# Optimization experiments

Measured on AMD Instinct MI355X. Metric: run time of the kernel, lower is better.

The kernel has to match this reference:

```python
import jax, jax.numpy as jnp
import numpy as np

B, L, D = 2, 256, 256  # batch, length, raw feature dim (W dims are D+1)

def setup_inputs() -> dict:
    key = jax.random.key(0)
    k1, k2, k3, kw = jax.random.split(key, 4)
    layer1 = jax.random.normal(k1, (B, L, D), dtype=jnp.float32)
    layer2 = jax.random.normal(k2, (B, L, D), dtype=jnp.float32)
    layer3 = jax.random.normal(k3, (B, L, D), dtype=jnp.float32)
    # xavier_normal_ for a 3D tensor: fan_in = D+1 * (D+1) receptive? torch treats
    # dim0 as fan_out-ish; we just use a matched-scale gaussian (correctness of the
    # contraction math is what matters for the kernel baseline).
    std = float(np.sqrt(2.0 / ((D + 1) + (D + 1) * (D + 1))))
    W = jax.random.normal(kw, (D + 1, D + 1, D + 1), dtype=jnp.float32) * std
    return {"layer1": layer1, "layer2": layer2, "layer3": layer3, "W": W}

def _append_ones(x):
    ones = jnp.ones(x.shape[:2] + (1,), dtype=x.dtype)
    return jnp.concatenate([x, ones], axis=-1)

def reference(layer1, layer2, layer3, W):
    l1 = _append_ones(layer1)  # [n, L, a]
    l2 = _append_ones(layer2)  # [n, L, b]
    l3 = _append_ones(layer3)  # [n, L, c]
    # Chained contraction: nia,abc -> nibc ; nibc,njb -> nijc ; nijc,nkc -> nijk
    t = jnp.einsum('nia,abc->nibc', l1, W)
    t = jnp.einsum('nibc,njb->nijc', t, l2)
    out = jnp.einsum('nijc,nkc->nijk', t, l3)
    return out
```

## Files before the change

kernel.cpp:

```cpp
#include <hip/hip_runtime.h>

typedef unsigned short u16;
typedef __attribute__((ext_vector_type(8))) short bf16x8;
typedef __attribute__((ext_vector_type(4))) float f32x4;

#define GLOAD_LDS16(gsrc, ldst)                                               \
  __builtin_amdgcn_global_load_lds(                                           \
      (const __attribute__((address_space(1))) void*)(gsrc),                  \
      (__attribute__((address_space(3))) void*)(ldst), 16, 0, 0)

#define LDSOFF(p) \
  ((unsigned)(uintptr_t)(__attribute__((address_space(3))) const void*)(p))

#define SB0 __builtin_amdgcn_sched_barrier(0)

__device__ __forceinline__ u16 f2bf(float x) {
  unsigned u = __float_as_uint(x);
  u = (u + 0x7FFFu + ((u >> 16) & 1u)) >> 16;
  return (u16)u;
}

__global__ void prep_l_kernel(const float* __restrict__ l1,
                              const float* __restrict__ l2,
                              const float* __restrict__ l3,
                              u16* __restrict__ o1, u16* __restrict__ o2,
                              u16* __restrict__ o3) {
  int idx = blockIdx.x * 256 + threadIdx.x;
  const int NR = 512 * 288;
  if (idx >= 3 * NR) return;
  int which = idx / NR, rem = idx - which * NR;
  int r = rem / 288, p = rem - r * 288;
  const float* s = which == 0 ? l1 : which == 1 ? l2 : l3;
  u16* d = which == 0 ? o1 : which == 1 ? o2 : o3;
  float v = (p < 256) ? s[r * 256 + p] : (p == 256 ? 1.0f : 0.0f);
  d[rem] = f2bf(v);
}

__global__ void prep_w_kernel(const float* __restrict__ W, u16* __restrict__ W2) {
  __shared__ float tile[32][33];
  const int a0 = blockIdx.x * 32, c0 = blockIdx.y * 32, b = blockIdx.z;
  const int t = threadIdx.x;
#pragma unroll
  for (int p = 0; p < 4; ++p) {
    int idx = t + p * 256;
    int cl = idx & 31, r = idx >> 5;
    int a = a0 + r, c = c0 + cl;
    float v = 0.0f;
    if (a < 257 && b < 257 && c < 257) v = W[((long)a * 257 + b) * 257 + c];
    tile[r][cl] = v;
  }
  __syncthreads();
#pragma unroll
  for (int p = 0; p < 4; ++p) {
    int idx = t + p * 256;
    int al = idx & 31, ccl = idx >> 5;
    W2[((long)(c0 + ccl) * 288 + b) * 288 + (a0 + al)] = f2bf(tile[al][ccl]);
  }
}

__global__ __launch_bounds__(256, 4) void gemm_nt(
    const u16* __restrict__ A, const u16* __restrict__ B, u16* __restrict__ C,
    int K, int lda, int ldb, int ldc) {
  __shared__ u16 As[2][4096];
  __shared__ u16 Bs[2][4096];
  const int t = threadIdx.x;
  const int bid = blockIdx.x;
  const int xcd = bid & 7, sq = bid >> 3;
  const int nt = xcd * 81 + (sq >> 2);
  const int mt = sq & 3;
  const int m0 = mt * 128, n0 = nt * 128;
  const int lane = t & 63;
  const int w = t >> 6;
  const int wr = (w >> 1) * 64, wc = (w & 1) * 64;
  const int r16 = lane & 15;
  const int cgrp = lane >> 4;
  const int rr = cgrp * 4;
  const unsigned ABase = LDSOFF(&As[0][0]);
  const unsigned BBase = LDSOFF(&Bs[0][0]);
  (void)K;

  const u16* PA = A + (long)m0 * lda;
  const u16* PB = B + (long)n0 * ldb;

#define STG(buf, k0)                                                          \
  {                                                                           \
    _Pragma("unroll") for (int _p = 0; _p < 2; ++_p) {                        \
      int _q = t + _p * 256;                                                  \
      int _r = _q >> 2, _g = (_q & 3) ^ ((_r >> 1) & 3);                      \
      GLOAD_LDS16(PA + (long)_r * lda + (k0) + _g * 8, &As[buf][_q * 8]);     \
      GLOAD_LDS16(PB + (long)_r * ldb + (k0) + _g * 8, &Bs[buf][_q * 8]);     \
    }                                                                         \
  }

  f32x4 acc[4][4];
  const f32x4 zero = {0.f, 0.f, 0.f, 0.f};
#pragma unroll
  for (int i = 0; i < 4; ++i)
#pragma unroll
    for (int j = 0; j < 4; ++j) acc[i][j] = zero;

  STG(0, 0);

#define GCOL(NI)                                                              \
  __builtin_amdgcn_s_setprio(1);                                              \
  acc[0][NI] = __builtin_amdgcn_mfma_f32_16x16x32_bf16(af[0], bf[NI], acc[0][NI], 0, 0, 0); \
  acc[1][NI] = __builtin_amdgcn_mfma_f32_16x16x32_bf16(af[1], bf[NI], acc[1][NI], 0, 0, 0); \
  acc[2][NI] = __builtin_amdgcn_mfma_f32_16x16x32_bf16(af[2], bf[NI], acc[2][NI], 0, 0, 0); \
  acc[3][NI] = __builtin_amdgcn_mfma_f32_16x16x32_bf16(af[3], bf[NI], acc[3][NI], 0, 0, 0); \
  __builtin_amdgcn_s_setprio(0);                                              \
  SB0;

#define GSTEP(KS, NW)                                                         \
  {                                                                           \
    if ((KS) < 8) STG(((KS) + 1) & 1, ((KS) + 1) * 32);                       \
    asm volatile("s_waitcnt vmcnt(" #NW ")" ::: "memory");                    \
    SB0;                                                                      \
    __builtin_amdgcn_s_barrier();                                             \
    SB0;                                                                      \
    bf16x8 af[4], bf[4];                                                      \
    _Pragma("unroll") for (int mi = 0; mi < 4; ++mi) {                        \
      int R = wr + mi * 16 + r16;                                             \
      unsigned ao = ABase + (unsigned)(((((KS) & 1) * 4096) + R * 32 +        \
                                       ((cgrp ^ ((R >> 1) & 3)) * 8)) * 2);   \
      asm volatile("ds_read_b128 %0, %1" : "=v"(af[mi]) : "v"(ao));           \
    }                                                                         \
    _Pragma("unroll") for (int ni = 0; ni < 4; ++ni) {                        \
      int R = wc + ni * 16 + r16;                                             \
      unsigned ao = BBase + (unsigned)(((((KS) & 1) * 4096) + R * 32 +        \
                                       ((cgrp ^ ((R >> 1) & 3)) * 8)) * 2);   \
      asm volatile("ds_read_b128 %0, %1" : "=v"(bf[ni]) : "v"(ao));           \
    }                                                                         \
    SB0;                                                                      \
    asm volatile("s_waitcnt lgkmcnt(3)" ::: "memory"); SB0;                   \
    GCOL(0)                                                                   \
    asm volatile("s_waitcnt lgkmcnt(2)" ::: "memory"); SB0;                   \
    GCOL(1)                                                                   \
    asm volatile("s_waitcnt lgkmcnt(1)" ::: "memory"); SB0;                   \
    GCOL(2)                                                                   \
    asm volatile("s_waitcnt lgkmcnt(0)" ::: "memory"); SB0;                   \
    GCOL(3)                                                                   \
  }

  GSTEP(0, 4) GSTEP(1, 4) GSTEP(2, 4) GSTEP(3, 4) GSTEP(4, 4)
  GSTEP(5, 4) GSTEP(6, 4) GSTEP(7, 4) GSTEP(8, 0)
#undef GSTEP
#undef GCOL
#undef STG

#pragma unroll
  for (int mi = 0; mi < 4; ++mi) {
    int gm = m0 + wr + mi * 16 + rr;
#pragma unroll
    for (int ni = 0; ni < 4; ++ni) {
      int gc = n0 + wc + ni * 16 + r16;
#pragma unroll
      for (int r = 0; r < 4; ++r)
        C[(long)(gm + r) * ldc + gc] = f2bf(acc[mi][ni][r]);
    }
  }
}

__global__ __launch_bounds__(512, 2) void fused23(
    const u16* __restrict__ l2b, const u16* __restrict__ l3b,
    const u16* __restrict__ T1, float* __restrict__ out) {
  __shared__ u16 S[128 * 296];
  __shared__ u16 Bst[4][288 * 32];
  const int t = threadIdx.x;
  const int lane = t & 63;
  const int w = t >> 6;

  const int bid = blockIdx.x;
  const int xcd = bid & 7;
  const int seq = bid >> 3;
  const int ni = xcd * 64 + (seq >> 1);
  const int half = seq & 1;
  const int n = ni >> 8;

  const int r16 = lane & 15;
  const int cgrp = lane >> 4;
  const int kb = cgrp * 8;
  const int rr = cgrp * 4;
  const f32x4 zero = {0.f, 0.f, 0.f, 0.f};

  const u16* A2 = l2b + (long)n * 73728 + (long)(half * 128) * 288;
  const u16* BT = T1 + (long)ni * 82944;
  const u16* B3 = l3b + (long)n * 73728;
  const unsigned BOF = LDSOFF(&Bst[0][0]);
  const unsigned SOF = LDSOFF(&S[0]);

#define ISSUE_A(buf, kk)                                                      \
  {                                                                           \
    int q1 = w * 144 + lane;                                                  \
    int r1 = q1 >> 2, g1 = (q1 & 3) ^ ((r1 >> 1) & 3);                        \
    GLOAD_LDS16(BT + (long)r1 * 288 + (kk) * 32 + g1 * 8, &Bst[(buf)][q1 * 8]); \
    int q2 = q1 + 64;                                                         \
    int r2 = q2 >> 2, g2 = (q2 & 3) ^ ((r2 >> 1) & 3);                        \
    GLOAD_LDS16(BT + (long)r2 * 288 + (kk) * 32 + g2 * 8, &Bst[(buf)][q2 * 8]); \
    if (lane < 16) {                                                          \
      int q3 = w * 144 + 128 + lane;                                          \
      int r3 = q3 >> 2, g3 = (q3 & 3) ^ ((r3 >> 1) & 3);                      \
      GLOAD_LDS16(BT + (long)r3 * 288 + (kk) * 32 + g3 * 8, &Bst[(buf)][q3 * 8]); \
    }                                                                         \
  }
#define ISSUE_B(buf, kk)                                                      \
  {                                                                           \
    int q1 = w * 128 + lane;                                                  \
    int r1 = q1 >> 2, g1 = (q1 & 3) ^ ((r1 >> 1) & 3);                        \
    GLOAD_LDS16(B3 + (long)r1 * 288 + (kk) * 32 + g1 * 8, &Bst[(buf)][q1 * 8]); \
    int q2 = q1 + 64;                                                         \
    int r2 = q2 >> 2, g2 = (q2 & 3) ^ ((r2 >> 1) & 3);                        \
    GLOAD_LDS16(B3 + (long)r2 * 288 + (kk) * 32 + g2 * 8, &Bst[(buf)][q2 * 8]); \
  }

  {
    const int wm = w & 3, wn = w >> 2;
    f32x4 acc[2][9];
#pragma unroll
    for (int i = 0; i < 2; ++i)
#pragma unroll
      for (int j = 0; j < 9; ++j) acc[i][j] = zero;

    bf16x8 afr[18];
#pragma unroll
    for (int k = 0; k < 9; ++k)
#pragma unroll
      for (int mi = 0; mi < 2; ++mi)
        afr[k * 2 + mi] = *(const bf16x8*)(A2 +
            (long)(wm * 32 + mi * 16 + r16) * 288 + k * 32 + kb);
    SB0;

    ISSUE_A(0, 0);
    ISSUE_A(1, 1);

#define FA_MM(NJ)                                                             \
  __builtin_amdgcn_s_setprio(1);                                              \
  acc[0][NJ] = __builtin_amdgcn_mfma_f32_16x16x32_bf16(afc0, bf[NJ], acc[0][NJ], 0, 0, 0); \
  acc[1][NJ] = __builtin_amdgcn_mfma_f32_16x16x32_bf16(afc1, bf[NJ], acc[1][NJ], 0, 0, 0); \
  __builtin_amdgcn_s_setprio(0);

#define FA_STEP(K, NW)                                                        \
  {                                                                           \
    if ((K) + 2 <= 8) ISSUE_A(((K) + 2) & 3, (K) + 2);                        \
    asm volatile("s_waitcnt vmcnt(" #NW ")" ::: "memory");                    \
    SB0;                                                                      \
    __builtin_amdgcn_s_barrier();                                             \
    SB0;                                                                      \
    bf16x8 bf[9];                                                             \
    _Pragma("unroll") for (int nj = 0; nj < 9; ++nj) {                        \
      const int R = wn * 144 + nj * 16 + r16;                                 \
      unsigned ao = BOF + (unsigned)((((K) & 3) * 9216 + R * 32 +             \
                                      ((cgrp ^ ((R >> 1) & 3)) * 8)) * 2);    \
      asm volatile("ds_read_b128 %0, %1" : "=v"(bf[nj]) : "v"(ao));           \
    }                                                                         \
    SB0;                                                                      \
    const bf16x8 afc0 = afr[(K) * 2 + 0], afc1 = afr[(K) * 2 + 1];            \
    asm volatile("s_waitcnt lgkmcnt(6)" ::: "memory"); SB0;                   \
    FA_MM(0) FA_MM(1) FA_MM(2) SB0;                                           \
    asm volatile("s_waitcnt lgkmcnt(3)" ::: "memory"); SB0;                   \
    FA_MM(3) FA_MM(4) FA_MM(5) SB0;                                           \
    asm volatile("s_waitcnt lgkmcnt(0)" ::: "memory"); SB0;                   \
    FA_MM(6) FA_MM(7) FA_MM(8) SB0;                                           \
  }
    FA_STEP(0, 6) FA_STEP(1, 6) FA_STEP(2, 6) FA_STEP(3, 6) FA_STEP(4, 6)
    FA_STEP(5, 6) FA_STEP(6, 6) FA_STEP(7, 3) FA_STEP(8, 0)
#undef FA_STEP
#undef FA_MM

    __syncthreads();
    ISSUE_B(0, 0);
    ISSUE_B(1, 1);
#pragma unroll
    for (int mi = 0; mi < 2; ++mi)
#pragma unroll
      for (int nj = 0; nj < 9; ++nj)
#pragma unroll
        for (int q = 0; q < 4; ++q)
          S[(wm * 32 + mi * 16 + rr + q) * 296 + wn * 144 + nj * 16 + r16] =
              f2bf(acc[mi][nj][q]);
  }
  __syncthreads();

  {
    const int wm = w & 1, wn = w >> 1;
    f32x4 acc[4][4];
#pragma unroll
    for (int i = 0; i < 4; ++i)
#pragma unroll
      for (int j = 0; j < 4; ++j) acc[i][j] = zero;

#define FB_MM(NI)                                                             \
  __builtin_amdgcn_s_setprio(1);                                              \
  acc[0][NI] = __builtin_amdgcn_mfma_f32_16x16x32_bf16(af[0], bf[NI], acc[0][NI], 0, 0, 0); \
  acc[1][NI] = __builtin_amdgcn_mfma_f32_16x16x32_bf16(af[1], bf[NI], acc[1][NI], 0, 0, 0); \
  acc[2][NI] = __builtin_amdgcn_mfma_f32_16x16x32_bf16(af[2], bf[NI], acc[2][NI], 0, 0, 0); \
  acc[3][NI] = __builtin_amdgcn_mfma_f32_16x16x32_bf16(af[3], bf[NI], acc[3][NI], 0, 0, 0); \
  __builtin_amdgcn_s_setprio(0);                                              \
  SB0;

#define FB_STEP(K, NW)                                                        \
  {                                                                           \
    if ((K) + 2 <= 8) ISSUE_B(((K) + 2) & 3, (K) + 2);                        \
    asm volatile("s_waitcnt vmcnt(" #NW ")" ::: "memory");                    \
    SB0;                                                                      \
    __builtin_amdgcn_s_barrier();                                             \
    SB0;                                                                      \
    bf16x8 af[4], bf[4];                                                      \
    _Pragma("unroll") for (int mi = 0; mi < 4; ++mi) {                        \
      unsigned ao = SOF + (unsigned)(((wm * 64 + mi * 16 + r16) * 296 +       \
                                      (K) * 32 + kb) * 2);                    \
      asm volatile("ds_read_b128 %0, %1" : "=v"(af[mi]) : "v"(ao));           \
    }                                                                         \
    _Pragma("unroll") for (int nj = 0; nj < 4; ++nj) {                        \
      const int R = wn * 64 + nj * 16 + r16;                                  \
      unsigned ao = BOF + (unsigned)((((K) & 3) * 9216 + R * 32 +             \
                                      ((cgrp ^ ((R >> 1) & 3)) * 8)) * 2);    \
      asm volatile("ds_read_b128 %0, %1" : "=v"(bf[nj]) : "v"(ao));           \
    }                                                                         \
    SB0;                                                                      \
    asm volatile("s_waitcnt lgkmcnt(3)" ::: "memory"); SB0;                   \
    FB_MM(0)                                                                  \
    asm volatile("s_waitcnt lgkmcnt(2)" ::: "memory"); SB0;                   \
    FB_MM(1)                                                                  \
    asm volatile("s_waitcnt lgkmcnt(1)" ::: "memory"); SB0;                   \
    FB_MM(2)                                                                  \
    asm volatile("s_waitcnt lgkmcnt(0)" ::: "memory"); SB0;                   \
    FB_MM(3)                                                                  \
  }
    FB_STEP(0, 4) FB_STEP(1, 4) FB_STEP(2, 4) FB_STEP(3, 4) FB_STEP(4, 4)
    FB_STEP(5, 4) FB_STEP(6, 4) FB_STEP(7, 2) FB_STEP(8, 0)
#undef FB_STEP
#undef FB_MM

    float* O = out + (long)ni * 65536 + (long)(half * 128 + wm * 64) * 256 + wn * 64;
#pragma unroll
    for (int mi = 0; mi < 4; ++mi)
#pragma unroll
      for (int nj = 0; nj < 4; ++nj)
#pragma unroll
        for (int q = 0; q < 4; ++q)
          O[(long)(mi * 16 + rr + q) * 256 + nj * 16 + r16] = acc[mi][nj][q];
  }
#undef ISSUE_A
#undef ISSUE_B
}

extern "C" void kernel_launch(void* const* d_in, const int* in_sizes, int n_in,
                              void* d_out, int out_size, void* d_ws, size_t ws_size,
                              hipStream_t stream) {
  const float* l1 = (const float*)d_in[0];
  const float* l2 = (const float*)d_in[1];
  const float* l3 = (const float*)d_in[2];
  const float* W = (const float*)d_in[3];
  float* out = (float*)d_out;
  char* ws = (char*)d_ws;

  const long LB = 512L * 288 * 2;
  u16* l1b = (u16*)ws;
  u16* l2b = (u16*)(ws + LB);
  u16* l3b = (u16*)(ws + 2 * LB);
  u16* T1 = (u16*)(ws + 3 * LB);
  u16* W2 = (u16*)d_out;

  prep_l_kernel<<<1728, 256, 0, stream>>>(l1, l2, l3, l1b, l2b, l3b);

  dim3 gw(9, 9, 288);
  prep_w_kernel<<<gw, 256, 0, stream>>>(W, W2);

  gemm_nt<<<2592, 256, 0, stream>>>(l1b, W2, T1, 288, 288, 288, 82944);

  fused23<<<1024, 512, 0, stream>>>(l2b, l3b, T1, out);
}
```

Baseline: 159.1 us.

## Enlarge gemm_nt tiles to 256x256 with 512 threads and reorder prefetch

The first GEMM now uses 256x256 output tiles computed by 8 waves, each producing a 128x64 sub-tile. This doubles operand reuse per LDS load and cuts the grid from 2592 to 648 blocks. The next k-slice prefetch is now issued after the current slice's LDS reads, with a full vmcnt(0) wait at the top of each step. The trade-offs are more accumulator registers, larger LDS buffers, fewer blocks for load balance, and less overlap between global loads and compute.

```diff
diff --git a/kernel.cpp b/kernel.cpp
--- a/kernel.cpp
+++ b/kernel.cpp
@@ -58,20 +58,21 @@
   }
 }
 
-__global__ __launch_bounds__(256, 4) void gemm_nt(
+__global__ __launch_bounds__(512, 2) void gemm_nt(
     const u16* __restrict__ A, const u16* __restrict__ B, u16* __restrict__ C,
     int K, int lda, int ldb, int ldc) {
-  __shared__ u16 As[2][4096];
-  __shared__ u16 Bs[2][4096];
+  __shared__ u16 As[2][8192];
+  __shared__ u16 Bs[2][8192];
   const int t = threadIdx.x;
   const int bid = blockIdx.x;
-  const int xcd = bid & 7, sq = bid >> 3;
-  const int nt = xcd * 81 + (sq >> 2);
-  const int mt = sq & 3;
-  const int m0 = mt * 128, n0 = nt * 128;
+  const int xcd = bid & 7, s = bid >> 3;
+  const int g = xcd * 81 + s;
+  const int mt = g & 1, nt = g >> 1;
+  const int m0 = mt * 256, n0 = nt * 256;
   const int lane = t & 63;
   const int w = t >> 6;
-  const int wr = (w >> 1) * 64, wc = (w & 1) * 64;
+  const int wm = w >> 2;
+  const int wn = w & 3;
   const int r16 = lane & 15;
   const int cgrp = lane >> 4;
   const int rr = cgrp * 4;
@@ -85,17 +86,17 @@
 #define STG(buf, k0)                                                          \
   {                                                                           \
     _Pragma("unroll") for (int _p = 0; _p < 2; ++_p) {                        \
-      int _q = t + _p * 256;                                                  \
+      int _q = t + _p * 512;                                                  \
       int _r = _q >> 2, _g = (_q & 3) ^ ((_r >> 1) & 3);                      \
       GLOAD_LDS16(PA + (long)_r * lda + (k0) + _g * 8, &As[buf][_q * 8]);     \
       GLOAD_LDS16(PB + (long)_r * ldb + (k0) + _g * 8, &Bs[buf][_q * 8]);     \
     }                                                                         \
   }
 
-  f32x4 acc[4][4];
+  f32x4 acc[8][4];
   const f32x4 zero = {0.f, 0.f, 0.f, 0.f};
 #pragma unroll
-  for (int i = 0; i < 4; ++i)
+  for (int i = 0; i < 8; ++i)
 #pragma unroll
     for (int j = 0; j < 4; ++j) acc[i][j] = zero;
 
@@ -103,33 +104,33 @@
 
 #define GCOL(NI)                                                              \
   __builtin_amdgcn_s_setprio(1);                                              \
-  acc[0][NI] = __builtin_amdgcn_mfma_f32_16x16x32_bf16(af[0], bf[NI], acc[0][NI], 0, 0, 0); \
-  acc[1][NI] = __builtin_amdgcn_mfma_f32_16x16x32_bf16(af[1], bf[NI], acc[1][NI], 0, 0, 0); \
-  acc[2][NI] = __builtin_amdgcn_mfma_f32_16x16x32_bf16(af[2], bf[NI], acc[2][NI], 0, 0, 0); \
-  acc[3][NI] = __builtin_amdgcn_mfma_f32_16x16x32_bf16(af[3], bf[NI], acc[3][NI], 0, 0, 0); \
+  _Pragma("unroll") for (int _mi = 0; _mi < 8; ++_mi)                         \
+    acc[_mi][NI] = __builtin_amdgcn_mfma_f32_16x16x32_bf16(                   \
+        af[_mi], bf[NI], acc[_mi][NI], 0, 0, 0);                              \
   __builtin_amdgcn_s_setprio(0);                                              \
   SB0;
 
-#define GSTEP(KS, NW)                                                         \
-  {                                                                           \
-    if ((KS) < 8) STG(((KS) + 1) & 1, ((KS) + 1) * 32);                       \
-    asm volatile("s_waitcnt vmcnt(" #NW ")" ::: "memory");                    \
+#define GSTEP(KS)                                                             \
+  {                                                                           \
+    asm volatile("s_waitcnt vmcnt(0)" ::: "memory");                          \
     SB0;                                                                      \
     __builtin_amdgcn_s_barrier();                                             \
     SB0;                                                                      \
-    bf16x8 af[4], bf[4];                                                      \
-    _Pragma("unroll") for (int mi = 0; mi < 4; ++mi) {                        \
-      int R = wr + mi * 16 + r16;                                             \
-      unsigned ao = ABase + (unsigned)(((((KS) & 1) * 4096) + R * 32 +        \
+    bf16x8 af[8], bf[4];                                                      \
+    _Pragma("unroll") for (int mi = 0; mi < 8; ++mi) {                        \
+      int R = wm * 128 + mi * 16 + r16;                                       \
+      unsigned ao = ABase + (unsigned)(((((KS) & 1) * 8192) + R * 32 +        \
                                        ((cgrp ^ ((R >> 1) & 3)) * 8)) * 2);   \
       asm volatile("ds_read_b128 %0, %1" : "=v"(af[mi]) : "v"(ao));           \
     }                                                                         \
     _Pragma("unroll") for (int ni = 0; ni < 4; ++ni) {                        \
-      int R = wc + ni * 16 + r16;                                             \
-      unsigned ao = BBase + (unsigned)(((((KS) & 1) * 4096) + R * 32 +        \
+      int R = wn * 64 + ni * 16 + r16;                                        \
+      unsigned ao = BBase + (unsigned)(((((KS) & 1) * 8192) + R * 32 +        \
                                        ((cgrp ^ ((R >> 1) & 3)) * 8)) * 2);   \
       asm volatile("ds_read_b128 %0, %1" : "=v"(bf[ni]) : "v"(ao));           \
     }                                                                         \
+    SB0;                                                                      \
+    if ((KS) < 8) STG(((KS) + 1) & 1, ((KS) + 1) * 32);                       \
     SB0;                                                                      \
     asm volatile("s_waitcnt lgkmcnt(3)" ::: "memory"); SB0;                   \
     GCOL(0)                                                                   \
@@ -141,18 +142,18 @@
     GCOL(3)                                                                   \
   }
 
-  GSTEP(0, 4) GSTEP(1, 4) GSTEP(2, 4) GSTEP(3, 4) GSTEP(4, 4)
-  GSTEP(5, 4) GSTEP(6, 4) GSTEP(7, 4) GSTEP(8, 0)
+  GSTEP(0) GSTEP(1) GSTEP(2) GSTEP(3) GSTEP(4)
+  GSTEP(5) GSTEP(6) GSTEP(7) GSTEP(8)
 #undef GSTEP
 #undef GCOL
 #undef STG
 
 #pragma unroll
-  for (int mi = 0; mi < 4; ++mi) {
-    int gm = m0 + wr + mi * 16 + rr;
+  for (int mi = 0; mi < 8; ++mi) {
+    int gm = m0 + wm * 128 + mi * 16 + rr;
 #pragma unroll
     for (int ni = 0; ni < 4; ++ni) {
-      int gc = n0 + wc + ni * 16 + r16;
+      int gc = n0 + wn * 64 + ni * 16 + r16;
 #pragma unroll
       for (int r = 0; r < 4; ++r)
         C[(long)(gm + r) * ldc + gc] = f2bf(acc[mi][ni][r]);
@@ -366,7 +367,7 @@
   dim3 gw(9, 9, 288);
   prep_w_kernel<<<gw, 256, 0, stream>>>(W, W2);
 
-  gemm_nt<<<2592, 256, 0, stream>>>(l1b, W2, T1, 288, 288, 288, 82944);
+  gemm_nt<<<648, 512, 0, stream>>>(l1b, W2, T1, 288, 288, 288, 82944);
 
   fused23<<<1024, 512, 0, stream>>>(l2b, l3b, T1, out);
 }
```

Result: no change. 159.2 us (+0.0%).
